# Performance work log

Hardware: AMD Instinct MI355X
Metric: run time of the kernel (lower is better)

## Reference

```python
import jax, jax.numpy as jnp
import numpy as np

MAX_LEN = 4096
HEAD_DIM = 128
NUM_HEAD = 32
NUM_KV_GROUPS = 8
NUM_HEAD_KV = NUM_HEAD // NUM_KV_GROUPS
BASE = 10000.0


def _rope_tables(seq_len):
    pos = jnp.arange(seq_len, dtype=jnp.float32)
    freq = BASE ** (-(jnp.arange(0, HEAD_DIM, 2, dtype=jnp.float32) / HEAD_DIM))
    ang = pos[:, None] * freq[None, :]  # [n, d/2]
    return jnp.cos(ang), jnp.sin(ang)


def _apply_rope(x, cos, sin):
    # x: [..., n, d]; interleaved even/odd rotation as in the torch RoPe
    even = x[..., ::2]
    odd = x[..., 1::2]
    even_r = even * cos - odd * sin
    odd_r = odd * cos + even * sin
    return jnp.stack([even_r, odd_r], axis=-1).reshape(x.shape)


def setup_inputs() -> dict:
    key = jax.random.key(0)
    ks = jax.random.split(key, 9)
    B, N, D = 4, 1024, NUM_HEAD * HEAD_DIM
    KV = NUM_HEAD_KV * HEAD_DIM
    s = 0.02
    return {
        "x": jax.random.normal(ks[0], (B, N, D), jnp.float32),
        "Wq": jax.random.normal(ks[1], (D, D), jnp.float32) * s,
        "bq": jax.random.normal(ks[2], (D,), jnp.float32) * s,
        "Wk": jax.random.normal(ks[3], (D, KV), jnp.float32) * s,
        "bk": jax.random.normal(ks[4], (KV,), jnp.float32) * s,
        "Wv": jax.random.normal(ks[5], (D, KV), jnp.float32) * s,
        "bv": jax.random.normal(ks[6], (KV,), jnp.float32) * s,
        "Wo": jax.random.normal(ks[7], (D, D), jnp.float32) * s,
        "bo": jax.random.normal(ks[8], (D,), jnp.float32) * s,
    }


def reference(x, Wq, bq, Wk, bk, Wv, bv, Wo, bo):
    B, N, _ = x.shape
    g, h, d = NUM_KV_GROUPS, NUM_HEAD_KV, HEAD_DIM
    scale = d ** (-0.5)

    q = x @ Wq + bq                      # [B, N, g*h*d]
    k = x @ Wk + bk                      # [B, N, h*d]
    v = x @ Wv + bv

    # b n (g h d) -> b g h n d (group-major, matching einops pattern)
    q = q.reshape(B, N, g, h, d).transpose(0, 2, 3, 1, 4)
    k = k.reshape(B, N, h, d).transpose(0, 2, 1, 3)   # b h n d
    v = v.reshape(B, N, h, d).transpose(0, 2, 1, 3)

    cos, sin = _rope_tables(N)
    q = _apply_rope(q, cos, sin)
    k = _apply_rope(k, cos, sin)

    attn = jnp.einsum('bghid,bhjd->bghij', q * scale, k)
    causal = jnp.tril(jnp.ones((N, N), dtype=bool))
    attn = jnp.where(causal, attn, -jnp.inf)
    attn = jax.nn.softmax(attn, axis=-1)

    out = jnp.einsum('bghij,bhjd->bghid', attn, v)
    out = out.transpose(0, 3, 1, 2, 4).reshape(B, N, g * h * d)  # b g h n d -> b n (g h d)
    return out @ Wo + bo
```

## Files before the change

### kernel.cpp

```cpp
#include <hip/hip_runtime.h>
#include <cstdint>
#include <cstddef>

typedef unsigned short u16;
typedef unsigned int u32;

typedef __bf16 bf16x8 __attribute__((ext_vector_type(8)));
typedef float f32x4 __attribute__((ext_vector_type(4)));

__device__ __forceinline__ u16 f2bf(float f) {
  union { float f; u32 u; } v; v.f = f;
  u32 r = v.u + 0x7fffu + ((v.u >> 16) & 1u);
  return (u16)(r >> 16);
}
__device__ __forceinline__ float bf2f(u16 h) {
  union { u32 u; float f; } v; v.u = ((u32)h) << 16;
  return v.f;
}

__device__ __forceinline__ void gld16(const u16* g, u16* l) {
  __builtin_amdgcn_global_load_lds((const __attribute__((address_space(1))) u32*)g,
                                   (__attribute__((address_space(3))) u32*)l,
                                   16, 0, 0);
}

template<bool OUT_F32>
__global__ __launch_bounds__(256)
void gemm_bt(const u16* __restrict__ A, const u16* __restrict__ Bt,
             const float* __restrict__ bias, void* __restrict__ C,
             int M, int N, int K) {
  __shared__ __attribute__((aligned(16))) u16 As[128*32];
  __shared__ __attribute__((aligned(16))) u16 Bs[128*32];
  const int tid  = threadIdx.x;
  const int lane = tid & 63;
  const int wave = tid >> 6;
  const int wm = wave >> 1, wn = wave & 1;
  const int bn = blockIdx.x * 128;
  const int bm = blockIdx.y * 128;
  const int kq = lane >> 4, ml = lane & 15;

  f32x4 acc[4][4] = {};

  for (int k0 = 0; k0 < K; k0 += 32) {
    __syncthreads();
#pragma unroll
    for (int j = 0; j < 2; ++j) {
      int s = wave*128 + j*64 + lane;
      int r = s >> 2;
      int c = (s & 3) ^ ((r >> 1) & 3);
      gld16(A  + (size_t)(bm + r)*K + k0 + c*8, As + (size_t)(wave*128 + j*64)*8);
      gld16(Bt + (size_t)(bn + r)*K + k0 + c*8, Bs + (size_t)(wave*128 + j*64)*8);
    }
    __syncthreads();
    bf16x8 af[4], bfr[4];
#pragma unroll
    for (int t = 0; t < 4; ++t) {
      int ra = wm*64 + t*16 + ml;
      af[t]  = *(const bf16x8*)(As + (size_t)(ra*4 + (kq ^ ((ra >> 1) & 3)))*8);
      int rb = wn*64 + t*16 + ml;
      bfr[t] = *(const bf16x8*)(Bs + (size_t)(rb*4 + (kq ^ ((rb >> 1) & 3)))*8);
    }
#pragma unroll
    for (int i = 0; i < 4; ++i)
#pragma unroll
      for (int j = 0; j < 4; ++j)
        acc[i][j] = __builtin_amdgcn_mfma_f32_16x16x32_bf16(af[i], bfr[j], acc[i][j], 0, 0, 0);
  }

#pragma unroll
  for (int i = 0; i < 4; ++i) {
    int rg0 = bm + wm*64 + i*16 + kq*4;
#pragma unroll
    for (int j = 0; j < 4; ++j) {
      int cg = bn + wn*64 + j*16 + ml;
      float bv = bias[cg];
#pragma unroll
      for (int r = 0; r < 4; ++r) {
        float v = acc[i][j][r] + bv;
        if (OUT_F32) ((float*)C)[(size_t)(rg0 + r)*N + cg] = v;
        else         ((u16*)C)[(size_t)(rg0 + r)*N + cg]   = f2bf(v);
      }
    }
  }
}

__global__ __launch_bounds__(256)
void attn(const u16* __restrict__ Q, const u16* __restrict__ K,
          const u16* __restrict__ V, u16* __restrict__ ctx) {
  __shared__ __attribute__((aligned(16))) u16 Qs[64*128];
  __shared__ __attribute__((aligned(16))) u16 Ks[64*128];
  __shared__ __attribute__((aligned(16))) u16 Vs[128*64];
  __shared__ __attribute__((aligned(16))) u16 Ps[4][16*72];
  const int qt  = blockIdx.x;
  const int bh  = blockIdx.y;
  const int b   = bh >> 5;
  const int kvh = bh & 3;
  const int tid = threadIdx.x;
  const int lane = tid & 63;
  const int wave = tid >> 6;
  const int kq = lane >> 4, ml = lane & 15;

  const u16* Qg = Q + ((size_t)bh*1024 + qt*64)*128;
  const u16* Kg = K + ((size_t)(b*4 + kvh))*1024*128;
  const u16* Vg = V + ((size_t)(b*4 + kvh))*128*1024;

#pragma unroll
  for (int j = 0; j < 4; ++j) {
    int s = wave*256 + j*64 + lane;
    int r = s >> 4, c = (s & 15) ^ (r & 7);
    gld16(Qg + (size_t)r*128 + c*8, Qs + (size_t)(wave*256 + j*64)*8);
  }

  f32x4 o[8] = {};
  float m_i[4] = {-1e30f, -1e30f, -1e30f, -1e30f};
  float l_i[4] = {0.f, 0.f, 0.f, 0.f};

  for (int kt = 0; kt <= qt; ++kt) {
    __syncthreads();
#pragma unroll
    for (int j = 0; j < 4; ++j) {
      int s = wave*256 + j*64 + lane;
      int r = s >> 4, c = (s & 15) ^ (r & 7);
      gld16(Kg + ((size_t)(kt*64 + r))*128 + c*8, Ks + (size_t)(wave*256 + j*64)*8);
    }
#pragma unroll
    for (int j = 0; j < 4; ++j) {
      int s = wave*256 + j*64 + lane;
      int d = s >> 3, c = (s & 7) ^ (d & 7);
      gld16(Vg + (size_t)d*1024 + kt*64 + c*8, Vs + (size_t)(wave*256 + j*64)*8);
    }
    __syncthreads();

    f32x4 sf[4] = {};
#pragma unroll
    for (int ks = 0; ks < 4; ++ks) {
      int rq = wave*16 + ml;
      int cq = ks*4 + kq;
      bf16x8 aq = *(const bf16x8*)(Qs + (size_t)(rq*16 + (cq ^ (rq & 7)))*8);
#pragma unroll
      for (int nt = 0; nt < 4; ++nt) {
        int rk = nt*16 + ml;
        bf16x8 bk = *(const bf16x8*)(Ks + (size_t)(rk*16 + (cq ^ (rk & 7)))*8);
        sf[nt] = __builtin_amdgcn_mfma_f32_16x16x32_bf16(aq, bk, sf[nt], 0, 0, 0);
      }
    }

    const int i0 = qt*64 + wave*16 + kq*4;
    if (kt == qt) {
#pragma unroll
      for (int nt = 0; nt < 4; ++nt) {
        int jg = kt*64 + nt*16 + ml;
#pragma unroll
        for (int r = 0; r < 4; ++r)
          if (jg > i0 + r) sf[nt][r] = -1e30f;
      }
    }
    float rmax[4] = {-1e30f, -1e30f, -1e30f, -1e30f};
#pragma unroll
    for (int nt = 0; nt < 4; ++nt)
#pragma unroll
      for (int r = 0; r < 4; ++r)
        rmax[r] = fmaxf(rmax[r], sf[nt][r]);
#pragma unroll
    for (int r = 0; r < 4; ++r) {
      float v = rmax[r];
      v = fmaxf(v, __shfl_xor(v, 1));
      v = fmaxf(v, __shfl_xor(v, 2));
      v = fmaxf(v, __shfl_xor(v, 4));
      v = fmaxf(v, __shfl_xor(v, 8));
      float mo = m_i[r];
      float mn = fmaxf(mo, v);
      m_i[r] = mn;
      rmax[r] = exp2f(mo - mn);
    }
    float rsum[4] = {0.f, 0.f, 0.f, 0.f};
#pragma unroll
    for (int nt = 0; nt < 4; ++nt)
#pragma unroll
      for (int r = 0; r < 4; ++r) {
        float p = exp2f(sf[nt][r] - m_i[r]);
        rsum[r] += p;
        Ps[wave][(kq*4 + r)*72 + nt*16 + ml] = f2bf(p);
      }
#pragma unroll
    for (int r = 0; r < 4; ++r) {
      float v = rsum[r];
      v += __shfl_xor(v, 1);
      v += __shfl_xor(v, 2);
      v += __shfl_xor(v, 4);
      v += __shfl_xor(v, 8);
      l_i[r] = l_i[r]*rmax[r] + v;
    }
#pragma unroll
    for (int dt = 0; dt < 8; ++dt)
#pragma unroll
      for (int r = 0; r < 4; ++r)
        o[dt][r] *= rmax[r];
    __syncthreads();

#pragma unroll
    for (int ks = 0; ks < 2; ++ks) {
      bf16x8 ap = *(const bf16x8*)(&Ps[wave][ml*72 + ks*32 + kq*8]);
#pragma unroll
      for (int dt = 0; dt < 8; ++dt) {
        int dv = dt*16 + ml;
        int cv = ks*4 + kq;
        bf16x8 bv = *(const bf16x8*)(Vs + (size_t)(dv*8 + (cv ^ (dv & 7)))*8);
        o[dt] = __builtin_amdgcn_mfma_f32_16x16x32_bf16(ap, bv, o[dt], 0, 0, 0);
      }
    }
  }

  const int head = bh & 31;
  float inv[4];
#pragma unroll
  for (int r = 0; r < 4; ++r) inv[r] = 1.f / l_i[r];
  size_t row0 = (size_t)b*1024 + qt*64 + wave*16 + kq*4;
#pragma unroll
  for (int dt = 0; dt < 8; ++dt) {
    int cg = head*128 + dt*16 + ml;
#pragma unroll
    for (int r = 0; r < 4; ++r)
      ctx[(row0 + r)*4096 + cg] = f2bf(o[dt][r]*inv[r]);
  }
}

__global__ void castx(const float* __restrict__ x, u16* __restrict__ xb) {
  size_t i = ((size_t)blockIdx.x*256 + threadIdx.x)*4;
  float4 v = *(const float4*)(x + i);
  u16 o0 = f2bf(v.x), o1 = f2bf(v.y), o2 = f2bf(v.z), o3 = f2bf(v.w);
  ushort4 o; o.x = o0; o.y = o1; o.z = o2; o.w = o3;
  *(ushort4*)(xb + i) = o;
}

__global__ void wtrans(const float* __restrict__ W, u16* __restrict__ Wt, int K, int N) {
  __shared__ u16 t[32][40];
  const int n0 = blockIdx.x*32, k0 = blockIdx.y*32;
  const int tid = threadIdx.x;
  const int r = tid >> 3, c4 = (tid & 7)*4;
  const float* src = W + (size_t)(k0 + r)*N + n0 + c4;
#pragma unroll
  for (int i = 0; i < 4; ++i) t[r][c4 + i] = f2bf(src[i]);
  __syncthreads();
  u16* dst = Wt + (size_t)(n0 + r)*K + k0 + c4;
#pragma unroll
  for (int i = 0; i < 4; ++i) dst[i] = t[c4 + i][r];
}

__global__ void packbias(const float* __restrict__ bq, const float* __restrict__ bk,
                         const float* __restrict__ bv, float* __restrict__ out) {
  int i = blockIdx.x*256 + threadIdx.x;
  float v;
  if (i < 4096)      v = bq[i];
  else if (i < 4608) v = bk[i - 4096];
  else               v = bv[i - 4608];
  out[i] = v;
}

__global__ void rope_q(const u16* __restrict__ qkv, u16* __restrict__ qr) {
  int idx = blockIdx.x*256 + threadIdx.x;
  int dp = idx & 63;
  int head = (idx >> 6) & 31;
  int n = (idx >> 11) & 1023;
  int b = idx >> 21;
  const u16* src = qkv + ((size_t)(b*1024 + n))*5120 + head*128 + dp*2;
  float e = bf2f(src[0]), od = bf2f(src[1]);
  float freq = exp2f((float)dp * -0.2076205059f);
  float ang = (float)n * freq;
  float c = cosf(ang), s = sinf(ang);
  const float QS = 0.12751747f;
  u16* dst = qr + (((size_t)(b*32 + head))*1024 + n)*128 + dp*2;
  dst[0] = f2bf((e*c - od*s)*QS);
  dst[1] = f2bf((od*c + e*s)*QS);
}

__global__ void rope_k(const u16* __restrict__ qkv, u16* __restrict__ kr) {
  int idx = blockIdx.x*256 + threadIdx.x;
  int dp = idx & 63;
  int kvh = (idx >> 6) & 3;
  int n = (idx >> 8) & 1023;
  int b = idx >> 18;
  const u16* src = qkv + ((size_t)(b*1024 + n))*5120 + 4096 + kvh*128 + dp*2;
  float e = bf2f(src[0]), od = bf2f(src[1]);
  float freq = exp2f((float)dp * -0.2076205059f);
  float ang = (float)n * freq;
  float c = cosf(ang), s = sinf(ang);
  u16* dst = kr + (((size_t)(b*4 + kvh))*1024 + n)*128 + dp*2;
  dst[0] = f2bf(e*c - od*s);
  dst[1] = f2bf(od*c + e*s);
}

__global__ void vtrans(const u16* __restrict__ qkv, u16* __restrict__ vt) {
  __shared__ u16 t[32][40];
  const int nt = blockIdx.x, dt = blockIdx.y, bk = blockIdx.z;
  const int b = bk >> 2, kvh = bk & 3;
  const int tid = threadIdx.x;
  const int r = tid >> 3, c4 = (tid & 7)*4;
  const u16* src = qkv + ((size_t)(b*1024 + nt*32 + r))*5120 + 4608 + kvh*128 + dt*32 + c4;
#pragma unroll
  for (int i = 0; i < 4; ++i) t[r][c4 + i] = src[i];
  __syncthreads();
  u16* dst = vt + ((size_t)((b*4 + kvh)*128 + dt*32 + r))*1024 + nt*32 + c4;
#pragma unroll
  for (int i = 0; i < 4; ++i) dst[i] = t[c4 + i][r];
}

extern "C" void kernel_launch(void* const* d_in, const int* in_sizes, int n_in,
                              void* d_out, int out_size, void* d_ws, size_t ws_size,
                              hipStream_t stream) {
  const float* x  = (const float*)d_in[0];
  const float* Wq = (const float*)d_in[1];
  const float* bq = (const float*)d_in[2];
  const float* Wk = (const float*)d_in[3];
  const float* bk = (const float*)d_in[4];
  const float* Wv = (const float*)d_in[5];
  const float* bv = (const float*)d_in[6];
  const float* Wo = (const float*)d_in[7];
  const float* bo = (const float*)d_in[8];
  float* out = (float*)d_out;

  char* ws = (char*)d_ws;
  u16*   xb   = (u16*)(ws + 0);
  u16*   wqkv = (u16*)(ws + 33554432);
  u16*   wo_t = (u16*)(ws + 75497472);
  float* bqkv = (float*)(ws + 109051904);
  u16*   qkvl = (u16*)(ws + 109072384);
  u16*   qr   = (u16*)(ws + 33554432);
  u16*   kr   = (u16*)(ws + 67108864);
  u16*   vt   = (u16*)(ws + 71303168);
  u16*   ctx  = (u16*)(ws + 0);

  castx<<<16384, 256, 0, stream>>>(x, xb);
  wtrans<<<dim3(128,128), 256, 0, stream>>>(Wq, wqkv, 4096, 4096);
  wtrans<<<dim3(16,128),  256, 0, stream>>>(Wk, wqkv + (size_t)4096*4096, 4096, 512);
  wtrans<<<dim3(16,128),  256, 0, stream>>>(Wv, wqkv + (size_t)4608*4096, 4096, 512);
  wtrans<<<dim3(128,128), 256, 0, stream>>>(Wo, wo_t, 4096, 4096);
  packbias<<<20, 256, 0, stream>>>(bq, bk, bv, bqkv);

  gemm_bt<false><<<dim3(40,32), 256, 0, stream>>>(xb, wqkv, bqkv, qkvl, 4096, 5120, 4096);

  rope_q<<<32768, 256, 0, stream>>>(qkvl, qr);
  rope_k<<<4096,  256, 0, stream>>>(qkvl, kr);
  vtrans<<<dim3(32,4,16), 256, 0, stream>>>(qkvl, vt);

  attn<<<dim3(16,128), 256, 0, stream>>>(qr, kr, vt, ctx);

  gemm_bt<true><<<dim3(32,32), 256, 0, stream>>>(ctx, wo_t, bo, out, 4096, 4096, 4096);
}
```

Baseline: 875.2 us.

## Double-buffer GEMM LDS loads, reverse attention tile order, vectorize weight transpose

The GEMM now uses two LDS buffers so the global-to-LDS load of the next K slice is issued before computing on the current one, with one barrier per slice instead of two. The attention grid visits query tiles in reverse, so the longest causal tiles are scheduled first. The weight transpose kernel works on 64x64 tiles with float4 loads and 16-byte stores. Together these aim to hide GEMM load latency, reduce the attention tail and cut transpose memory traffic, at the cost of doubled GEMM LDS use, which could lower occupancy.

```diff
diff --git a/kernel.cpp b/kernel.cpp
--- a/kernel.cpp
+++ b/kernel.cpp
@@ -7,6 +7,7 @@
 
 typedef __bf16 bf16x8 __attribute__((ext_vector_type(8)));
 typedef float f32x4 __attribute__((ext_vector_type(4)));
+typedef u16 u16x8 __attribute__((ext_vector_type(8)));
 
 __device__ __forceinline__ u16 f2bf(float f) {
   union { float f; u32 u; } v; v.f = f;
@@ -29,8 +30,8 @@
 void gemm_bt(const u16* __restrict__ A, const u16* __restrict__ Bt,
              const float* __restrict__ bias, void* __restrict__ C,
              int M, int N, int K) {
-  __shared__ __attribute__((aligned(16))) u16 As[128*32];
-  __shared__ __attribute__((aligned(16))) u16 Bs[128*32];
+  __shared__ __attribute__((aligned(16))) u16 As[2][128*32];
+  __shared__ __attribute__((aligned(16))) u16 Bs[2][128*32];
   const int tid  = threadIdx.x;
   const int lane = tid & 63;
   const int wave = tid >> 6;
@@ -39,32 +40,51 @@
   const int bm = blockIdx.y * 128;
   const int kq = lane >> 4, ml = lane & 15;
 
+  const u16* agp[2]; const u16* bgp[2]; int ldst[2];
+#pragma unroll
+  for (int j = 0; j < 2; ++j) {
+    int s = wave*128 + j*64 + lane;
+    int r = s >> 2;
+    int c = (s & 3) ^ ((r >> 1) & 3);
+    agp[j] = A  + (size_t)(bm + r)*K + c*8;
+    bgp[j] = Bt + (size_t)(bn + r)*K + c*8;
+    ldst[j] = (wave*128 + j*64)*8;
+  }
+
+  auto stage = [&](int p, int k0) {
+#pragma unroll
+    for (int j = 0; j < 2; ++j) {
+      gld16(agp[j] + k0, &As[p][0] + ldst[j]);
+      gld16(bgp[j] + k0, &Bs[p][0] + ldst[j]);
+    }
+  };
+
   f32x4 acc[4][4] = {};
 
-  for (int k0 = 0; k0 < K; k0 += 32) {
-    __syncthreads();
-#pragma unroll
-    for (int j = 0; j < 2; ++j) {
-      int s = wave*128 + j*64 + lane;
-      int r = s >> 2;
-      int c = (s & 3) ^ ((r >> 1) & 3);
-      gld16(A  + (size_t)(bm + r)*K + k0 + c*8, As + (size_t)(wave*128 + j*64)*8);
-      gld16(Bt + (size_t)(bn + r)*K + k0 + c*8, Bs + (size_t)(wave*128 + j*64)*8);
-    }
-    __syncthreads();
+  auto compute = [&](int p) {
     bf16x8 af[4], bfr[4];
 #pragma unroll
     for (int t = 0; t < 4; ++t) {
       int ra = wm*64 + t*16 + ml;
-      af[t]  = *(const bf16x8*)(As + (size_t)(ra*4 + (kq ^ ((ra >> 1) & 3)))*8);
+      af[t]  = *(const bf16x8*)(&As[p][0] + (size_t)(ra*4 + (kq ^ ((ra >> 1) & 3)))*8);
       int rb = wn*64 + t*16 + ml;
-      bfr[t] = *(const bf16x8*)(Bs + (size_t)(rb*4 + (kq ^ ((rb >> 1) & 3)))*8);
+      bfr[t] = *(const bf16x8*)(&Bs[p][0] + (size_t)(rb*4 + (kq ^ ((rb >> 1) & 3)))*8);
     }
 #pragma unroll
     for (int i = 0; i < 4; ++i)
 #pragma unroll
       for (int j = 0; j < 4; ++j)
         acc[i][j] = __builtin_amdgcn_mfma_f32_16x16x32_bf16(af[i], bfr[j], acc[i][j], 0, 0, 0);
+  };
+
+  stage(0, 0);
+  for (int k0 = 0; k0 < K; k0 += 64) {
+    __syncthreads();
+    if (k0 + 32 < K) stage(1, k0 + 32);
+    compute(0);
+    __syncthreads();
+    if (k0 + 64 < K) stage(0, k0 + 64);
+    compute(1);
   }
 
 #pragma unroll
@@ -91,7 +111,7 @@
   __shared__ __attribute__((aligned(16))) u16 Ks[64*128];
   __shared__ __attribute__((aligned(16))) u16 Vs[128*64];
   __shared__ __attribute__((aligned(16))) u16 Ps[4][16*72];
-  const int qt  = blockIdx.x;
+  const int qt  = (int)gridDim.x - 1 - (int)blockIdx.x;
   const int bh  = blockIdx.y;
   const int b   = bh >> 5;
   const int kvh = bh & 3;
@@ -228,23 +248,31 @@
 __global__ void castx(const float* __restrict__ x, u16* __restrict__ xb) {
   size_t i = ((size_t)blockIdx.x*256 + threadIdx.x)*4;
   float4 v = *(const float4*)(x + i);
-  u16 o0 = f2bf(v.x), o1 = f2bf(v.y), o2 = f2bf(v.z), o3 = f2bf(v.w);
-  ushort4 o; o.x = o0; o.y = o1; o.z = o2; o.w = o3;
+  ushort4 o; o.x = f2bf(v.x); o.y = f2bf(v.y); o.z = f2bf(v.z); o.w = f2bf(v.w);
   *(ushort4*)(xb + i) = o;
 }
 
 __global__ void wtrans(const float* __restrict__ W, u16* __restrict__ Wt, int K, int N) {
-  __shared__ u16 t[32][40];
-  const int n0 = blockIdx.x*32, k0 = blockIdx.y*32;
+  __shared__ u16 t[64*71 + 8];
+  const int n0 = blockIdx.x*64, k0 = blockIdx.y*64;
   const int tid = threadIdx.x;
-  const int r = tid >> 3, c4 = (tid & 7)*4;
-  const float* src = W + (size_t)(k0 + r)*N + n0 + c4;
-#pragma unroll
-  for (int i = 0; i < 4; ++i) t[r][c4 + i] = f2bf(src[i]);
+  const int kr = tid >> 4, nc = (tid & 15)*4;
+#pragma unroll
+  for (int i = 0; i < 4; ++i) {
+    float4 v = *(const float4*)(W + (size_t)(k0 + kr + i*16)*N + n0 + nc);
+    u16* d = &t[(kr + i*16)*71 + nc];
+    d[0] = f2bf(v.x); d[1] = f2bf(v.y); d[2] = f2bf(v.z); d[3] = f2bf(v.w);
+  }
   __syncthreads();
-  u16* dst = Wt + (size_t)(n0 + r)*K + k0 + c4;
-#pragma unroll
-  for (int i = 0; i < 4; ++i) dst[i] = t[c4 + i][r];
+  const int n = tid >> 2, k16 = (tid & 3)*16;
+  u16x8 lo, hi;
+#pragma unroll
+  for (int j = 0; j < 8; ++j) lo[j] = t[(k16 + j)*71 + n];
+#pragma unroll
+  for (int j = 0; j < 8; ++j) hi[j] = t[(k16 + 8 + j)*71 + n];
+  u16* dst = Wt + (size_t)(n0 + n)*K + k0 + k16;
+  *(u16x8*)(dst)     = lo;
+  *(u16x8*)(dst + 8) = hi;
 }
 
 __global__ void packbias(const float* __restrict__ bq, const float* __restrict__ bk,
@@ -331,10 +359,10 @@
   u16*   ctx  = (u16*)(ws + 0);
 
   castx<<<16384, 256, 0, stream>>>(x, xb);
-  wtrans<<<dim3(128,128), 256, 0, stream>>>(Wq, wqkv, 4096, 4096);
-  wtrans<<<dim3(16,128),  256, 0, stream>>>(Wk, wqkv + (size_t)4096*4096, 4096, 512);
-  wtrans<<<dim3(16,128),  256, 0, stream>>>(Wv, wqkv + (size_t)4608*4096, 4096, 512);
-  wtrans<<<dim3(128,128), 256, 0, stream>>>(Wo, wo_t, 4096, 4096);
+  wtrans<<<dim3(64,64), 256, 0, stream>>>(Wq, wqkv, 4096, 4096);
+  wtrans<<<dim3(8,64),  256, 0, stream>>>(Wk, wqkv + (size_t)4096*4096, 4096, 512);
+  wtrans<<<dim3(8,64),  256, 0, stream>>>(Wv, wqkv + (size_t)4608*4096, 4096, 512);
+  wtrans<<<dim3(64,64), 256, 0, stream>>>(Wo, wo_t, 4096, 4096);
   packbias<<<20, 256, 0, stream>>>(bq, bk, bv, bqkv);
 
   gemm_bt<false><<<dim3(40,32), 256, 0, stream>>>(xb, wqkv, bqkv, qkvl, 4096, 5120, 4096);
```

New measurement: 838.8 us. -4.2%, faster.
